# Optimization experiments

Measured on AMD Instinct MI355X. Metric: run time of the kernel, lower is better.

## Reference

```python
import jax, jax.numpy as jnp
import numpy as np

R = 8192   # rows of the input matrix (attention sequence dim)
F = 4096   # total input feature columns
L = 2048   # number of gathered columns (len(in_keys))


def setup_inputs() -> dict:
    key = jax.random.key(0)
    k1, k2, k3 = jax.random.split(key, 3)
    inputs = jax.random.normal(k1, (R, F), dtype=jnp.float32)
    in_idxs = jax.random.randint(k2, (L,), 0, F)
    weights = jax.random.normal(k3, (L, 3), dtype=jnp.float32)
    return {"inputs": inputs, "in_idxs": in_idxs, "weights": weights}


def reference(inputs, in_idxs, weights):
    # gather: torch.index_select(inputs, 1, in_idxs) -> [R, L]
    sel = jnp.take(inputs, in_idxs, axis=1)
    # QKV projection: [R, L] @ [L, 3] -> [R, 3]; chunk -> q, k, v each [R, 1]
    qkv = sel @ weights
    q, k, v = qkv[:, 0:1], qkv[:, 1:2], qkv[:, 2:3]
    d_k = q.shape[-1]  # = 1
    # scaled dot-product attention over the row dim: logits [R, R]
    logits = (q @ k.T) / jnp.sqrt(jnp.float32(d_k))
    attn = jax.nn.softmax(logits, axis=-1)
    values = attn @ v  # [R, 1]
    # out = activation(values[-1:, ]) -> [1, 1]
    return jax.nn.sigmoid(values[-1:, :])
```

## Files before the change

### kernel.cpp

```cpp
#include <hip/hip_runtime.h>
#include <math.h>

#define RR 8192
#define FF 4096
#define LL 2048
#define RPB 8
#define NBLK (RR / RPB)

#define WS_W1 0
#define WS_W2 FF
#define WS_Q  (2 * FF)
#define WS_P  (2 * FF + 1)

__global__ __launch_bounds__(1024) void prep(const float* __restrict__ in,
                                             const int* __restrict__ idx,
                                             const float* __restrict__ wts,
                                             float* __restrict__ ws) {
    __shared__ float w1s[FF];
    __shared__ float w2s[FF];
    __shared__ float qred[16];

    const int t = threadIdx.x, lane = t & 63, wv = t >> 6;

    for (int i = t; i < FF; i += 1024) { w1s[i] = 0.f; w2s[i] = 0.f; }
    __syncthreads();

    const float* lastrow = in + (size_t)(RR - 1) * FF;
    float qp = 0.f;
#pragma unroll
    for (int l = t; l < LL; l += 1024) {
        const int c = idx[l];
        qp += lastrow[c] * wts[3 * l + 0];
        atomicAdd(&w1s[c], wts[3 * l + 1]);
        atomicAdd(&w2s[c], wts[3 * l + 2]);
    }
    for (int o = 32; o > 0; o >>= 1) qp += __shfl_down(qp, o);
    if (lane == 0) qred[wv] = qp;
    __syncthreads();

    if (t < FF / 4) {
        *(float4*)(ws + WS_W1 + t * 4) = *(const float4*)&w1s[t * 4];
        *(float4*)(ws + WS_W2 + t * 4) = *(const float4*)&w2s[t * 4];
    }
    if (t == 0) {
        float q = 0.f;
#pragma unroll
        for (int i = 0; i < 16; ++i) q += qred[i];
        ws[WS_Q] = q;
    }
}

__global__ __launch_bounds__(512) void gemv_kv(const float* __restrict__ in,
                                               const float* __restrict__ ws,
                                               float* __restrict__ partials) {
    const int t = threadIdx.x, lane = t & 63, wv = t >> 6;
    const int row = blockIdx.x * RPB + wv;
    const float* __restrict__ x  = in + (size_t)row * FF;
    const float* __restrict__ w1 = ws + WS_W1;
    const float* __restrict__ w2 = ws + WS_W2;

    float k = 0.f, v = 0.f;
#pragma unroll
    for (int i = 0; i < FF; i += 256) {
        const int c = i + lane * 4;
        const float4 xv = *(const float4*)(x + c);
        const float4 a1 = *(const float4*)(w1 + c);
        const float4 a2 = *(const float4*)(w2 + c);
        k += xv.x * a1.x + xv.y * a1.y + xv.z * a1.z + xv.w * a1.w;
        v += xv.x * a2.x + xv.y * a2.y + xv.z * a2.z + xv.w * a2.w;
    }
    for (int o = 32; o > 0; o >>= 1) { k += __shfl_down(k, o); v += __shfl_down(v, o); }

    __shared__ float kv[RPB][2];
    if (lane == 0) { kv[wv][0] = k; kv[wv][1] = v; }
    __syncthreads();

    if (t == 0) {
        const float q = ws[WS_Q];
        float m = -INFINITY;
#pragma unroll
        for (int r = 0; r < RPB; ++r) m = fmaxf(m, q * kv[r][0]);
        float se = 0.f, sv = 0.f;
#pragma unroll
        for (int r = 0; r < RPB; ++r) {
            const float e = expf(q * kv[r][0] - m);
            se += e;
            sv += e * kv[r][1];
        }
        partials[blockIdx.x * 3 + 0] = m;
        partials[blockIdx.x * 3 + 1] = se;
        partials[blockIdx.x * 3 + 2] = sv;
    }
}

__global__ __launch_bounds__(256) void combine(const float* __restrict__ partials,
                                               float* __restrict__ out) {
    const int t = threadIdx.x, lane = t & 63, wv = t >> 6;
    float lm[NBLK / 256], lse[NBLK / 256], lsv[NBLK / 256];
    float m = -INFINITY;
#pragma unroll
    for (int i = 0; i < NBLK / 256; ++i) {
        const int b = t + i * 256;
        lm[i]  = partials[b * 3 + 0];
        lse[i] = partials[b * 3 + 1];
        lsv[i] = partials[b * 3 + 2];
        m = fmaxf(m, lm[i]);
    }

    __shared__ float red[4], red2[4], red3[4], bcast[1];
    for (int o = 32; o > 0; o >>= 1) m = fmaxf(m, __shfl_down(m, o));
    if (lane == 0) red[wv] = m;
    __syncthreads();
    if (t == 0) bcast[0] = fmaxf(fmaxf(red[0], red[1]), fmaxf(red[2], red[3]));
    __syncthreads();
    const float gm = bcast[0];

    float se = 0.f, sv = 0.f;
#pragma unroll
    for (int i = 0; i < NBLK / 256; ++i) {
        const float s = expf(lm[i] - gm);
        se += lse[i] * s;
        sv += lsv[i] * s;
    }
    for (int o = 32; o > 0; o >>= 1) { se += __shfl_down(se, o); sv += __shfl_down(sv, o); }
    if (lane == 0) { red2[wv] = se; red3[wv] = sv; }
    __syncthreads();
    if (t == 0) {
        const float S = red2[0] + red2[1] + red2[2] + red2[3];
        const float V = red3[0] + red3[1] + red3[2] + red3[3];
        const float val = V / S;
        out[0] = 1.0f / (1.0f + expf(-val));
    }
}

extern "C" void kernel_launch(void* const* d_in, const int* in_sizes, int n_in,
                              void* d_out, int out_size, void* d_ws, size_t ws_size,
                              hipStream_t stream) {
    const float* inputs = (const float*)d_in[0];
    const int*   idx    = (const int*)d_in[1];
    const float* wts    = (const float*)d_in[2];
    float* out = (float*)d_out;
    float* ws  = (float*)d_ws;

    prep<<<1, 1024, 0, stream>>>(inputs, idx, wts, ws);
    gemv_kv<<<NBLK, 512, 0, stream>>>(inputs, ws, ws + WS_P);
    combine<<<1, 256, 0, stream>>>(ws + WS_P, out);
}
```

Measured before the change: 35.55 us.

## Fuse combine into GEMV via last-block atomic counter and stage weights in LDS

Merges the separate combine kernel into the GEMV kernel: each block publishes its softmax partials with agent-scope atomic stores, bumps a global counter, and the last block to finish performs the final reduction and sigmoid. This removes one kernel launch and its inter-kernel gap. Each block also copies the two folded weight vectors into shared memory before the row dot products, replacing repeated global/L2 weight loads with LDS reads at the cost of 32KB LDS per block, which may lower occupancy, plus an upfront copy and barrier.

```diff
diff --git a/kernel.cpp b/kernel.cpp
--- a/kernel.cpp
+++ b/kernel.cpp
@@ -4,13 +4,14 @@
 #define RR 8192
 #define FF 4096
 #define LL 2048
-#define RPB 8
-#define NBLK (RR / RPB)
+#define TPB 512
+#define NBLK (RR / 8)
 
-#define WS_W1 0
-#define WS_W2 FF
-#define WS_Q  (2 * FF)
-#define WS_P  (2 * FF + 1)
+#define WS_W1  0
+#define WS_W2  FF
+#define WS_Q   (2 * FF)
+#define WS_CNT (2 * FF + 4)
+#define WS_P   (2 * FF + 16)
 
 __global__ __launch_bounds__(1024) void prep(const float* __restrict__ in,
                                              const int* __restrict__ idx,
@@ -47,31 +48,40 @@
 #pragma unroll
         for (int i = 0; i < 16; ++i) q += qred[i];
         ws[WS_Q] = q;
+        *((unsigned int*)(ws + WS_CNT)) = 0u;
     }
 }
 
-__global__ __launch_bounds__(512) void gemv_kv(const float* __restrict__ in,
-                                               const float* __restrict__ ws,
-                                               float* __restrict__ partials) {
+__global__ __launch_bounds__(TPB) void gemv_combine(const float* __restrict__ in,
+                                                    float* __restrict__ ws,
+                                                    float* __restrict__ out) {
+    __shared__ float w1s[FF];
+    __shared__ float w2s[FF];
+    __shared__ float kv[8][2];
+    __shared__ int lastFlag;
+    __shared__ float red[8], red2[8], red3[8], bc[1];
+
     const int t = threadIdx.x, lane = t & 63, wv = t >> 6;
-    const int row = blockIdx.x * RPB + wv;
-    const float* __restrict__ x  = in + (size_t)row * FF;
-    const float* __restrict__ w1 = ws + WS_W1;
-    const float* __restrict__ w2 = ws + WS_W2;
 
+    for (int i = t; i < FF / 4; i += TPB) {
+        *(float4*)&w1s[i * 4] = *(const float4*)(ws + WS_W1 + i * 4);
+        *(float4*)&w2s[i * 4] = *(const float4*)(ws + WS_W2 + i * 4);
+    }
+    __syncthreads();
+
+    const int row = blockIdx.x * 8 + wv;
+    const float* __restrict__ x = in + (size_t)row * FF;
     float k = 0.f, v = 0.f;
 #pragma unroll
     for (int i = 0; i < FF; i += 256) {
         const int c = i + lane * 4;
         const float4 xv = *(const float4*)(x + c);
-        const float4 a1 = *(const float4*)(w1 + c);
-        const float4 a2 = *(const float4*)(w2 + c);
+        const float4 a1 = *(const float4*)&w1s[c];
+        const float4 a2 = *(const float4*)&w2s[c];
         k += xv.x * a1.x + xv.y * a1.y + xv.z * a1.z + xv.w * a1.w;
         v += xv.x * a2.x + xv.y * a2.y + xv.z * a2.z + xv.w * a2.w;
     }
     for (int o = 32; o > 0; o >>= 1) { k += __shfl_down(k, o); v += __shfl_down(v, o); }
-
-    __shared__ float kv[RPB][2];
     if (lane == 0) { kv[wv][0] = k; kv[wv][1] = v; }
     __syncthreads();
 
@@ -79,45 +89,52 @@
         const float q = ws[WS_Q];
         float m = -INFINITY;
 #pragma unroll
-        for (int r = 0; r < RPB; ++r) m = fmaxf(m, q * kv[r][0]);
+        for (int r = 0; r < 8; ++r) m = fmaxf(m, q * kv[r][0]);
         float se = 0.f, sv = 0.f;
 #pragma unroll
-        for (int r = 0; r < RPB; ++r) {
+        for (int r = 0; r < 8; ++r) {
             const float e = expf(q * kv[r][0] - m);
             se += e;
             sv += e * kv[r][1];
         }
-        partials[blockIdx.x * 3 + 0] = m;
-        partials[blockIdx.x * 3 + 1] = se;
-        partials[blockIdx.x * 3 + 2] = sv;
+        float* p = ws + WS_P + blockIdx.x * 3;
+        __hip_atomic_store(p + 0, m,  __ATOMIC_RELAXED, __HIP_MEMORY_SCOPE_AGENT);
+        __hip_atomic_store(p + 1, se, __ATOMIC_RELAXED, __HIP_MEMORY_SCOPE_AGENT);
+        __hip_atomic_store(p + 2, sv, __ATOMIC_RELAXED, __HIP_MEMORY_SCOPE_AGENT);
+        __threadfence();
+        const unsigned old = atomicAdd((unsigned int*)(ws + WS_CNT), 1u);
+        lastFlag = (old == NBLK - 1) ? 1 : 0;
     }
-}
+    __syncthreads();
+    if (!lastFlag) return;
 
-__global__ __launch_bounds__(256) void combine(const float* __restrict__ partials,
-                                               float* __restrict__ out) {
-    const int t = threadIdx.x, lane = t & 63, wv = t >> 6;
-    float lm[NBLK / 256], lse[NBLK / 256], lsv[NBLK / 256];
+    __threadfence();
+    const float* __restrict__ P = ws + WS_P;
+    float lm[NBLK / TPB], lse[NBLK / TPB], lsv[NBLK / TPB];
     float m = -INFINITY;
 #pragma unroll
-    for (int i = 0; i < NBLK / 256; ++i) {
-        const int b = t + i * 256;
-        lm[i]  = partials[b * 3 + 0];
-        lse[i] = partials[b * 3 + 1];
-        lsv[i] = partials[b * 3 + 2];
+    for (int i = 0; i < NBLK / TPB; ++i) {
+        const int b = t + i * TPB;
+        lm[i]  = __hip_atomic_load(P + b * 3 + 0, __ATOMIC_RELAXED, __HIP_MEMORY_SCOPE_AGENT);
+        lse[i] = __hip_atomic_load(P + b * 3 + 1, __ATOMIC_RELAXED, __HIP_MEMORY_SCOPE_AGENT);
+        lsv[i] = __hip_atomic_load(P + b * 3 + 2, __ATOMIC_RELAXED, __HIP_MEMORY_SCOPE_AGENT);
         m = fmaxf(m, lm[i]);
     }
-
-    __shared__ float red[4], red2[4], red3[4], bcast[1];
     for (int o = 32; o > 0; o >>= 1) m = fmaxf(m, __shfl_down(m, o));
     if (lane == 0) red[wv] = m;
     __syncthreads();
-    if (t == 0) bcast[0] = fmaxf(fmaxf(red[0], red[1]), fmaxf(red[2], red[3]));
+    if (t == 0) {
+        float x = red[0];
+#pragma unroll
+        for (int i = 1; i < 8; ++i) x = fmaxf(x, red[i]);
+        bc[0] = x;
+    }
     __syncthreads();
-    const float gm = bcast[0];
+    const float gm = bc[0];
 
     float se = 0.f, sv = 0.f;
 #pragma unroll
-    for (int i = 0; i < NBLK / 256; ++i) {
+    for (int i = 0; i < NBLK / TPB; ++i) {
         const float s = expf(lm[i] - gm);
         se += lse[i] * s;
         sv += lsv[i] * s;
@@ -126,10 +143,10 @@
     if (lane == 0) { red2[wv] = se; red3[wv] = sv; }
     __syncthreads();
     if (t == 0) {
-        const float S = red2[0] + red2[1] + red2[2] + red2[3];
-        const float V = red3[0] + red3[1] + red3[2] + red3[3];
-        const float val = V / S;
-        out[0] = 1.0f / (1.0f + expf(-val));
+        float S = 0.f, V = 0.f;
+#pragma unroll
+        for (int i = 0; i < 8; ++i) { S += red2[i]; V += red3[i]; }
+        out[0] = 1.0f / (1.0f + expf(-(V / S)));
     }
 }
 
@@ -143,6 +160,5 @@
     float* ws  = (float*)d_ws;
 
     prep<<<1, 1024, 0, stream>>>(inputs, idx, wts, ws);
-    gemv_kv<<<NBLK, 512, 0, stream>>>(inputs, ws, ws + WS_P);
-    combine<<<1, 256, 0, stream>>>(ws + WS_P, out);
+    gemv_combine<<<NBLK, TPB, 0, stream>>>(inputs, ws, out);
 }
```

New measurement: 66.27 us. 86.4% more time.
